# Kernel optimization log

Hardware: AMD Instinct MI355X
Metric: run time of the kernel (lower is better)

## Reference

```python
import jax, jax.numpy as jnp
import numpy as np

B, T, S, H, V, L = 64, 60, 60, 512, 32000, 2
NEG = -1.0e9  # matches torch mask value -1000000000.0


def setup_inputs() -> dict:
    key = jax.random.key(0)
    ks = jax.random.split(key, 12)
    sc = 0.05
    return {
        "indices": jax.random.randint(ks[0], (B, T), 0, V),
        "enc_output": jax.random.normal(ks[1], (B, S, H), dtype=jnp.float32),
        "de_lens": jax.random.randint(ks[2], (B,), 1, S + 1),
        "emb": jax.random.normal(ks[3], (V, H), dtype=jnp.float32) * sc,
        "w_ih": jax.random.normal(ks[4], (L, 4 * H, H), dtype=jnp.float32) * sc,
        "w_hh": jax.random.normal(ks[5], (L, 4 * H, H), dtype=jnp.float32) * sc,
        "b_ih": jnp.zeros((L, 4 * H), dtype=jnp.float32),
        "b_hh": jnp.zeros((L, 4 * H), dtype=jnp.float32),
        "lin_w": jax.random.normal(ks[6], (L, H, 2 * H), dtype=jnp.float32) * sc,
        "lin_b": jnp.zeros((L, H), dtype=jnp.float32),
        "out_w": jax.random.normal(ks[7], (V, H), dtype=jnp.float32) * sc,
        "out_b": jnp.zeros((V,), dtype=jnp.float32),
    }


def _lstm_seq(x, w_ih, w_hh, b_ih, b_hh):
    # x: [B,T,H] -> hidden states [B,T,H]; torch gate order i,f,g,o
    xg = jnp.einsum('bth,gh->btg', x, w_ih) + b_ih  # [B,T,4H]
    h0 = jnp.zeros((x.shape[0], w_hh.shape[1]), x.dtype)

    def step(carry, xg_t):
        h, c = carry
        g = xg_t + h @ w_hh.T + b_hh
        i, f, gg, o = jnp.split(g, 4, axis=-1)
        c = jax.nn.sigmoid(f) * c + jax.nn.sigmoid(i) * jnp.tanh(gg)
        h = jax.nn.sigmoid(o) * jnp.tanh(c)
        return (h, c), h

    _, hs = jax.lax.scan(step, (h0, h0), jnp.swapaxes(xg, 0, 1))
    return jnp.swapaxes(hs, 0, 1)


def reference(indices, enc_output, de_lens, emb, w_ih, w_hh, b_ih, b_hh,
              lin_w, lin_b, out_w, out_b):
    # additive length mask over encoder positions: [B,S]
    mask = jnp.where(jnp.arange(S)[None, :] < de_lens[:, None], 0.0, NEG).astype(enc_output.dtype)
    x = emb[indices]  # [B,T,H]
    for l in range(L):
        dec = _lstm_seq(x, w_ih[l], w_hh[l], b_ih[l], b_hh[l])  # [B,T,H]
        scores = jnp.einsum('bth,bsh->bts', dec, enc_output) + mask[:, None, :]
        probs = jax.nn.softmax(scores, axis=-1)
        attn = jnp.einsum('bts,bsh->bth', probs, enc_output)
        cat = jnp.concatenate([dec, attn], axis=-1)  # [B,T,2H]
        x = jnp.einsum('btk,hk->bth', cat, lin_w[l]) + lin_b[l]
    return jnp.einsum('bth,vh->btv', x, out_w) + out_b  # [B,T,V]
```

## Files before the change

### kernel.cpp

```cpp
#include <hip/hip_runtime.h>
#include <hip/hip_bf16.h>
#include <math.h>

#define B_ 64
#define T_ 60
#define S_ 60
#define H_ 512
#define V_ 32000
#define L_ 2
#define BT_ (B_*T_)
#define LDSROW2 72

typedef __attribute__((ext_vector_type(8))) short short8;
typedef __attribute__((ext_vector_type(4))) float f32x4;
typedef __attribute__((ext_vector_type(4))) unsigned int u32x4;

__device__ __forceinline__ short f2bf(float x) {
  __hip_bfloat16 h = __float2bfloat16(x);
  return __builtin_bit_cast(short, h);
}
__device__ __forceinline__ float bf2f(short s) {
  unsigned int u = ((unsigned int)(unsigned short)s) << 16;
  return __builtin_bit_cast(float, u);
}
__device__ __forceinline__ float sigm(float x) { return 1.f / (1.f + __expf(-x)); }
__device__ __forceinline__ float tanh_(float x) {
  float e = __expf(-2.f * fabsf(x));
  float t = (1.f - e) / (1.f + e);
  return x >= 0.f ? t : -t;
}

__device__ __forceinline__ void ld4g(const char* p, u32x4* q, bool llc) {
  if (llc)
    asm volatile("global_load_dwordx4 %0, %4, off sc0 sc1\n\t"
                 "global_load_dwordx4 %1, %4, off offset:16 sc0 sc1\n\t"
                 "global_load_dwordx4 %2, %4, off offset:32 sc0 sc1\n\t"
                 "global_load_dwordx4 %3, %4, off offset:48 sc0 sc1"
                 : "=v"(q[0]), "=v"(q[1]), "=v"(q[2]), "=v"(q[3]) : "v"(p));
  else
    asm volatile("global_load_dwordx4 %0, %4, off sc0\n\t"
                 "global_load_dwordx4 %1, %4, off offset:16 sc0\n\t"
                 "global_load_dwordx4 %2, %4, off offset:32 sc0\n\t"
                 "global_load_dwordx4 %3, %4, off offset:48 sc0"
                 : "=v"(q[0]), "=v"(q[1]), "=v"(q[2]), "=v"(q[3]) : "v"(p));
}

#define LDSBAR() do { \
    asm volatile("s_waitcnt lgkmcnt(0)" ::: "memory"); \
    __builtin_amdgcn_s_barrier(); \
    __builtin_amdgcn_sched_barrier(0); \
  } while (0)

__global__ __launch_bounds__(256) void convbf_k(const float* __restrict__ src,
                                                short* __restrict__ dst) {
  int g = blockIdx.x * 256 + threadIdx.x;
  const float* s = src + (size_t)g * 8;
  float4 v0 = *(const float4*)s, v1 = *(const float4*)(s + 4);
  short8 o;
  o[0]=f2bf(v0.x); o[1]=f2bf(v0.y); o[2]=f2bf(v0.z); o[3]=f2bf(v0.w);
  o[4]=f2bf(v1.x); o[5]=f2bf(v1.y); o[6]=f2bf(v1.z); o[7]=f2bf(v1.w);
  *(short8*)(dst + (size_t)g * 8) = o;
}

__global__ __launch_bounds__(256) void pack_whh_k(const float* __restrict__ whh,
                                                  short* __restrict__ pk) {
  int idx = blockIdx.x * 256 + threadIdx.x;
  int l = idx >> 17, rem = idx & 131071;
  int n = rem >> 6, k8 = rem & 63;
  int g = n >> 9, j = n & 511;
  int np = (j >> 4) * 64 + g * 16 + (j & 15);
  const float* src = whh + ((size_t)l * 2048 + n) * 512 + k8 * 8;
  float4 v0 = *(const float4*)src, v1 = *(const float4*)(src + 4);
  short8 o;
  o[0]=f2bf(v0.x); o[1]=f2bf(v0.y); o[2]=f2bf(v0.z); o[3]=f2bf(v0.w);
  o[4]=f2bf(v1.x); o[5]=f2bf(v1.y); o[6]=f2bf(v1.z); o[7]=f2bf(v1.w);
  size_t dst = (size_t)l * (2048 * 512) + ((size_t)((np >> 4) * 64 + k8)) * 128 + (np & 15) * 8;
  *(short8*)(pk + dst) = o;
}

__global__ __launch_bounds__(256) void embed_k(const int* __restrict__ idx,
                                               const float* __restrict__ emb,
                                               short* __restrict__ xhi,
                                               short* __restrict__ xlo) {
  int e = blockIdx.x * 256 + threadIdx.x;
  int bt = e >> 9, h = e & (H_ - 1);
  int row = idx[bt];
  float v = emb[(size_t)row * H_ + h];
  short hi = f2bf(v);
  xhi[e] = hi;
  xlo[e] = f2bf(v - bf2f(hi));
}

template<bool XPOSE>
__global__ __launch_bounds__(256) void gemm_hl_k(
    const short* __restrict__ Ahi, const short* __restrict__ Alo,
    const short* __restrict__ Bbf,
    const float* __restrict__ bias1, const float* __restrict__ bias2,
    float* __restrict__ C, short* __restrict__ Chi, short* __restrict__ Clo,
    int M, int N, int K) {
  __shared__ short Ahs[128 * LDSROW2];
  __shared__ short Als[128 * LDSROW2];
  __shared__ short Bs[128 * LDSROW2];
  int tid = threadIdx.x;
  int bm = blockIdx.y * 128, bn = blockIdx.x * 128;
  int wid = tid >> 6, lane = tid & 63;
  int wr = wid >> 1, wc = wid & 1;
  int lrow = lane & 15;
  f32x4 acc[4][4];
#pragma unroll
  for (int i = 0; i < 4; ++i)
#pragma unroll
    for (int j = 0; j < 4; ++j) acc[i][j] = (f32x4){0.f, 0.f, 0.f, 0.f};

  int srow = tid >> 1, scol = (tid & 1) * 32;

  for (int k0 = 0; k0 < K; k0 += 64) {
    const short* ahp = Ahi + (size_t)(bm + srow) * K + k0 + scol;
    const short* alp = Alo + (size_t)(bm + srow) * K + k0 + scol;
    const short* bp  = Bbf + (size_t)(bn + srow) * K + k0 + scol;
#pragma unroll
    for (int u = 0; u < 4; ++u) {
      *(short8*)(Ahs + srow * LDSROW2 + scol + u * 8) = *(const short8*)(ahp + u * 8);
      *(short8*)(Als + srow * LDSROW2 + scol + u * 8) = *(const short8*)(alp + u * 8);
      *(short8*)(Bs  + srow * LDSROW2 + scol + u * 8) = *(const short8*)(bp  + u * 8);
    }
    __syncthreads();
#pragma unroll
    for (int kk = 0; kk < 2; ++kk) {
      int lk = kk * 32 + (lane >> 4) * 8;
      short8 ah[4], al[4], bfr[4];
#pragma unroll
      for (int i = 0; i < 4; ++i) {
        ah[i] = *(const short8*)(Ahs + (wr * 64 + i * 16 + lrow) * LDSROW2 + lk);
        al[i] = *(const short8*)(Als + (wr * 64 + i * 16 + lrow) * LDSROW2 + lk);
      }
#pragma unroll
      for (int j = 0; j < 4; ++j)
        bfr[j] = *(const short8*)(Bs + (wc * 64 + j * 16 + lrow) * LDSROW2 + lk);
#pragma unroll
      for (int i = 0; i < 4; ++i)
#pragma unroll
        for (int j = 0; j < 4; ++j) {
          acc[i][j] = __builtin_amdgcn_mfma_f32_16x16x32_bf16(ah[i], bfr[j], acc[i][j], 0, 0, 0);
          acc[i][j] = __builtin_amdgcn_mfma_f32_16x16x32_bf16(al[i], bfr[j], acc[i][j], 0, 0, 0);
        }
    }
    __syncthreads();
  }

#pragma unroll
  for (int j = 0; j < 4; ++j) {
    int col = bn + wc * 64 + j * 16 + lrow;
    float bv = bias1[col] + (bias2 ? bias2[col] : 0.f);
#pragma unroll
    for (int i = 0; i < 4; ++i) {
#pragma unroll
      for (int r = 0; r < 4; ++r) {
        int row = bm + wr * 64 + i * 16 + (lane >> 4) * 4 + r;
        float v = acc[i][j][r] + bv;
        if (XPOSE) {
          int b = row / T_, t = row - b * T_;
          int g = col >> 9, jg = col & 511;
          int c8 = b >> 3, bloc = b & 7, q = jg >> 6;
          int nploc = ((jg >> 4) & 3) * 64 + g * 16 + (jg & 15);
          C[(((size_t)t * 64 + q * 8 + c8) * 8 + bloc) * 256 + nploc] = v;
        } else {
          short hi = f2bf(v);
          Chi[(size_t)row * N + col] = hi;
          Clo[(size_t)row * N + col] = f2bf(v - bf2f(hi));
        }
      }
    }
  }
}

__global__ __launch_bounds__(256) void gemm_bb_k(
    const short* __restrict__ A, const short* __restrict__ Bbf,
    const float* __restrict__ bias, float* __restrict__ C) {
  const int N = V_, K = H_;
  int n = blockIdx.x;
  int xcd = n & 7, pos = n >> 3;
  int base = (xcd < 4) ? xcd * 938 : 4 * 938 + (xcd - 4) * 937;
  int wg = base + pos;
  int bm = (wg % 30) * 128;
  int bn = (wg / 30) * 128;

  __shared__ short As[128 * LDSROW2];
  __shared__ short Bs[128 * LDSROW2];
  int tid = threadIdx.x;
  int wid = tid >> 6, lane = tid & 63;
  int wr = wid >> 1, wc = wid & 1;
  int lrow = lane & 15;
  f32x4 acc[4][4];
#pragma unroll
  for (int i = 0; i < 4; ++i)
#pragma unroll
    for (int j = 0; j < 4; ++j) acc[i][j] = (f32x4){0.f, 0.f, 0.f, 0.f};

  int srow = tid >> 2, scol = (tid & 3) * 16;

  for (int k0 = 0; k0 < K; k0 += 64) {
#pragma unroll
    for (int it = 0; it < 2; ++it) {
      int r = srow + it * 64;
      const short* ap = A + (size_t)(bm + r) * K + k0 + scol;
      short8 a0 = *(const short8*)ap, a1 = *(const short8*)(ap + 8);
      *(short8*)(As + r * LDSROW2 + scol) = a0;
      *(short8*)(As + r * LDSROW2 + scol + 8) = a1;
      const short* bp = Bbf + (size_t)(bn + r) * K + k0 + scol;
      short8 b0 = *(const short8*)bp, b1 = *(const short8*)(bp + 8);
      *(short8*)(Bs + r * LDSROW2 + scol) = b0;
      *(short8*)(Bs + r * LDSROW2 + scol + 8) = b1;
    }
    __syncthreads();
#pragma unroll
    for (int kk = 0; kk < 2; ++kk) {
      int lk = kk * 32 + (lane >> 4) * 8;
      short8 af[4], bfr[4];
#pragma unroll
      for (int i = 0; i < 4; ++i)
        af[i] = *(const short8*)(As + (wr * 64 + i * 16 + lrow) * LDSROW2 + lk);
#pragma unroll
      for (int j = 0; j < 4; ++j)
        bfr[j] = *(const short8*)(Bs + (wc * 64 + j * 16 + lrow) * LDSROW2 + lk);
#pragma unroll
      for (int i = 0; i < 4; ++i)
#pragma unroll
        for (int j = 0; j < 4; ++j)
          acc[i][j] = __builtin_amdgcn_mfma_f32_16x16x32_bf16(af[i], bfr[j], acc[i][j], 0, 0, 0);
    }
    __syncthreads();
  }

#pragma unroll
  for (int j = 0; j < 4; ++j) {
    int col = bn + wc * 64 + j * 16 + lrow;
    float bv = bias[col];
#pragma unroll
    for (int i = 0; i < 4; ++i)
#pragma unroll
      for (int r = 0; r < 4; ++r) {
        int row = bm + wr * 64 + i * 16 + (lane >> 4) * 4 + r;
        float v = acc[i][j][r] + bv;
        float* cp = C + (size_t)row * N + col;
        asm volatile("global_store_dword %0, %1, off nt" :: "v"(cp), "v"(v) : "memory");
      }
  }
}

__global__ __launch_bounds__(512, 2) void lstm_seq_k(
    const float* __restrict__ xg,
    const short* __restrict__ whh_pk,
    char* __restrict__ hx,
    float* __restrict__ dec) {
  __shared__ short hhi[16][520];
  __shared__ short hlo[16][520];
  __shared__ float gates[256][20];
  const int tid = threadIdx.x;
  const int bid = blockIdx.x;
  const int c = bid & 7, q = bid >> 3;
  const int w = tid >> 6, lane = tid & 63;
  const int lr = lane & 15, lkg = lane >> 4;

  for (int i = tid; i < 16 * 520; i += 512) {
    ((short*)hhi)[i] = 0;
    ((short*)hlo)[i] = 0;
  }

  short8 wreg[2][16];
#pragma unroll
  for (int nt = 0; nt < 2; ++nt)
#pragma unroll
    for (int kt = 0; kt < 16; ++kt)
      wreg[nt][kt] = *(const short8*)(whh_pk +
          ((size_t)((q * 16 + w * 2 + nt) * 64 + kt * 4 + lkg)) * 128 + lr * 8);

  const bool epi = (tid < 256);
  const int bloc_e = tid & 7;
  const int p_e = (tid >> 3) & 31;
  const int j0 = p_e * 2;
  const int s = tid & 255;
  char* grp = hx + (size_t)c * 65536;

  float cc0 = 0.f, cc1 = 0.f;
  __syncthreads();

  for (int t = 0; t < T_; ++t) {
    const unsigned tgt = (unsigned)t;
    float2 xgv[4];
    const int rw0 = (j0 >> 4) * 64 + (j0 & 15);
    if (epi) {
      const float* xb = xg + ((size_t)t * 64 + bid) * 2048 + bloc_e * 256;
#pragma unroll
      for (int g = 0; g < 4; ++g) xgv[g] = *(const float2*)(xb + rw0 + g * 16);
      asm volatile("" ::: "memory");
    } else {
      const char* base = grp + (size_t)(t & 1) * 32768;
      const char* pA = base + (size_t)s * 64;
      const char* pB = base + (size_t)(s + 256) * 64;
      u32x4 qA[4], qB[4];
      ld4g(pA, qA, true);
      ld4g(pB, qB, true);
      for (;;) {
        asm volatile("s_waitcnt vmcnt(0)" ::: "memory");
        __builtin_amdgcn_sched_barrier(0);
        unsigned bad = 0;
#pragma unroll
        for (int i = 0; i < 4; ++i) bad |= (qA[i][2] ^ tgt) | (qB[i][2] ^ tgt);
        if (!bad) break;
        __builtin_amdgcn_s_sleep(1);
        ld4g(pA, qA, true);
        ld4g(pB, qB, true);
      }
      u32x4 hA = {qA[0][0], qA[1][0], qA[2][0], qA[3][0]};
      u32x4 lA = {qA[0][1], qA[1][1], qA[2][1], qA[3][1]};
      u32x4 hB = {qB[0][0], qB[1][0], qB[2][0], qB[3][0]};
      u32x4 lB = {qB[0][1], qB[1][1], qB[2][1], qB[3][1]};
      *(u32x4*)(&hhi[s >> 6][(s & 63) * 8]) = hA;
      *(u32x4*)(&hlo[s >> 6][(s & 63) * 8]) = lA;
      *(u32x4*)(&hhi[4 + (s >> 6)][(s & 63) * 8]) = hB;
      *(u32x4*)(&hlo[4 + (s >> 6)][(s & 63) * 8]) = lB;
    }
    LDSBAR();

    f32x4 acc[2];
    acc[0] = (f32x4){0.f, 0.f, 0.f, 0.f};
    acc[1] = (f32x4){0.f, 0.f, 0.f, 0.f};
#pragma unroll
    for (int kt = 0; kt < 16; ++kt) {
      short8 ah = *(const short8*)(&hhi[lr][kt * 32 + lkg * 8]);
      short8 al = *(const short8*)(&hlo[lr][kt * 32 + lkg * 8]);
#pragma unroll
      for (int nt = 0; nt < 2; ++nt) {
        acc[nt] = __builtin_amdgcn_mfma_f32_16x16x32_bf16(ah, wreg[nt][kt], acc[nt], 0, 0, 0);
        acc[nt] = __builtin_amdgcn_mfma_f32_16x16x32_bf16(al, wreg[nt][kt], acc[nt], 0, 0, 0);
      }
    }
#pragma unroll
    for (int nt = 0; nt < 2; ++nt)
      *(f32x4*)(&gates[(w * 2 + nt) * 16 + lr][lkg * 4]) = acc[nt];
    LDSBAR();

    if (epi) {
      float gv0[4], gv1[4];
#pragma unroll
      for (int g = 0; g < 4; ++g) {
        int rw = rw0 + g * 16;
        gv0[g] = gates[rw][bloc_e] + xgv[g].x;
        gv1[g] = gates[rw + 1][bloc_e] + xgv[g].y;
      }
      float cn0 = sigm(gv0[1]) * cc0 + sigm(gv0[0]) * tanh_(gv0[2]);
      float hn0 = sigm(gv0[3]) * tanh_(cn0);
      cc0 = cn0;
      float cn1 = sigm(gv1[1]) * cc1 + sigm(gv1[0]) * tanh_(gv1[2]);
      float hn1 = sigm(gv1[3]) * tanh_(cn1);
      cc1 = cn1;
      short hi0 = f2bf(hn0), hi1 = f2bf(hn1);
      short lo0 = f2bf(hn0 - bf2f(hi0)), lo1 = f2bf(hn1 - bf2f(hi1));
      u32x4 hv;
      hv[0] = (unsigned)(unsigned short)hi0 | ((unsigned)(unsigned short)hi1 << 16);
      hv[1] = (unsigned)(unsigned short)lo0 | ((unsigned)(unsigned short)lo1 << 16);
      hv[2] = tgt + 1u;
      hv[3] = tgt + 1u;
      char* pb = grp + (size_t)((t + 1) & 1) * 32768 +
                 ((size_t)(bloc_e * 256 + q * 32 + p_e)) * 16;
      asm volatile("global_store_dwordx4 %0, %1, off sc0" :: "v"(pb), "v"(hv) : "memory");
      asm volatile("global_store_dwordx4 %0, %1, off sc0 sc1" :: "v"(pb), "v"(hv) : "memory");
      float2 dv; dv.x = hn0; dv.y = hn1;
      *(float2*)(dec + ((size_t)(c * 8 + bloc_e) * T_ + t) * H_ + q * 64 + j0) = dv;
    }
    LDSBAR();
  }
}

__global__ __launch_bounds__(256) void attn_k(const float* __restrict__ dec,
                                              const float* __restrict__ enc,
                                              const int* __restrict__ lens,
                                              short* __restrict__ cat_hi,
                                              short* __restrict__ cat_lo) {
  int bt = blockIdx.x;
  int b = bt / T_;
  __shared__ float dsh[H_];
  __shared__ float p[64];
  int tid = threadIdx.x;
  dsh[tid] = dec[(size_t)bt * H_ + tid];
  dsh[tid + 256] = dec[(size_t)bt * H_ + tid + 256];
  __syncthreads();
  int wid = tid >> 6, lane = tid & 63;
  int len = lens[b];
  for (int s = wid; s < S_; s += 4) {
    const float* er = enc + ((size_t)(b * S_ + s)) * H_ + lane * 8;
    float4 e0 = *(const float4*)er, e1 = *(const float4*)(er + 4);
    const float* dr = dsh + lane * 8;
    float sum = e0.x*dr[0] + e0.y*dr[1] + e0.z*dr[2] + e0.w*dr[3]
              + e1.x*dr[4] + e1.y*dr[5] + e1.z*dr[6] + e1.w*dr[7];
#pragma unroll
    for (int off = 32; off > 0; off >>= 1) sum += __shfl_down(sum, off);
    if (lane == 0) p[s] = sum + (s < len ? 0.f : -1.0e9f);
  }
  __syncthreads();
  if (wid == 0) {
    float v = (lane < S_) ? p[lane] : -INFINITY;
    float m = v;
#pragma unroll
    for (int off = 32; off > 0; off >>= 1) m = fmaxf(m, __shfl_down(m, off));
    m = __shfl(m, 0);
    float e = (lane < S_) ? expf(v - m) : 0.f;
    float ssum = e;
#pragma unroll
    for (int off = 32; off > 0; off >>= 1) ssum += __shfl_down(ssum, off);
    ssum = __shfl(ssum, 0);
    if (lane < S_) p[lane] = e / ssum;
  }
  __syncthreads();
  int h = tid * 2;
  float a0 = 0.f, a1 = 0.f;
  for (int s = 0; s < S_; ++s) {
    float ps = p[s];
    const float* er = enc + ((size_t)(b * S_ + s)) * H_ + h;
    a0 += ps * er[0];
    a1 += ps * er[1];
  }
  size_t base = (size_t)bt * (2 * H_);
  float vv[4] = {dsh[h], dsh[h + 1], a0, a1};
  int   oo[4] = {h, h + 1, H_ + h, H_ + h + 1};
#pragma unroll
  for (int i = 0; i < 4; ++i) {
    short hi = f2bf(vv[i]);
    cat_hi[base + oo[i]] = hi;
    cat_lo[base + oo[i]] = f2bf(vv[i] - bf2f(hi));
  }
}

extern "C" void kernel_launch(void* const* d_in, const int* in_sizes, int n_in,
                              void* d_out, int out_size, void* d_ws, size_t ws_size,
                              hipStream_t stream) {
  (void)in_sizes; (void)n_in; (void)out_size; (void)ws_size;
  const int*   indices = (const int*)d_in[0];
  const float* enc     = (const float*)d_in[1];
  const int*   de_lens = (const int*)d_in[2];
  const float* emb     = (const float*)d_in[3];
  const float* w_ih    = (const float*)d_in[4];
  const float* w_hh    = (const float*)d_in[5];
  const float* b_ih    = (const float*)d_in[6];
  const float* b_hh    = (const float*)d_in[7];
  const float* lin_w   = (const float*)d_in[8];
  const float* lin_b   = (const float*)d_in[9];
  const float* out_w   = (const float*)d_in[10];
  const float* out_b   = (const float*)d_in[11];
  float* outp = (float*)d_out;

  char* ws = (char*)d_ws;
  size_t off = 0;
  auto alloc = [&](size_t bytes) -> void* {
    void* p = ws + off; off += (bytes + 255) & ~(size_t)255; return p;
  };
  short* x_hi   = (short*)alloc((size_t)BT_ * H_ * 2);
  short* x_lo   = (short*)alloc((size_t)BT_ * H_ * 2);
  float* xg     = (float*)alloc((size_t)BT_ * 4 * H_ * 4);
  float* dec    = (float*)alloc((size_t)BT_ * H_ * 4);
  short* cat_hi = (short*)alloc((size_t)BT_ * 2 * H_ * 2);
  short* cat_lo = (short*)alloc((size_t)BT_ * 2 * H_ * 2);
  short* ow_bf  = (short*)alloc((size_t)V_ * H_ * 2);
  short* wih_bf = (short*)alloc((size_t)L_ * 4 * H_ * H_ * 2);
  short* linw_bf= (short*)alloc((size_t)L_ * H_ * 2 * H_ * 2);
  short* whh_pk = (short*)alloc((size_t)L_ * 4 * H_ * H_ * 2);
  char*  hx     = (char*)alloc((size_t)8 * 2 * 32768);

  convbf_k<<<V_ * H_ / 8 / 256, 256, 0, stream>>>(out_w, ow_bf);
  convbf_k<<<L_ * 4 * H_ * H_ / 8 / 256, 256, 0, stream>>>(w_ih, wih_bf);
  convbf_k<<<L_ * H_ * 2 * H_ / 8 / 256, 256, 0, stream>>>(lin_w, linw_bf);
  pack_whh_k<<<L_ * 2048 * 64 / 256, 256, 0, stream>>>(w_hh, whh_pk);
  embed_k<<<BT_ * H_ / 256, 256, 0, stream>>>(indices, emb, x_hi, x_lo);

  for (int l = 0; l < L_; ++l) {
    gemm_hl_k<true><<<dim3(4 * H_ / 128, BT_ / 128), 256, 0, stream>>>(
        x_hi, x_lo, wih_bf + (size_t)l * 4 * H_ * H_,
        b_ih + l * 4 * H_, b_hh + l * 4 * H_,
        xg, nullptr, nullptr, BT_, 4 * H_, H_);
    hipMemsetAsync(hx, 0, (size_t)8 * 2 * 32768, stream);
    lstm_seq_k<<<64, 512, 0, stream>>>(
        xg, whh_pk + (size_t)l * 4 * H_ * H_, hx, dec);
    attn_k<<<BT_, 256, 0, stream>>>(dec, enc, de_lens, cat_hi, cat_lo);
    gemm_hl_k<false><<<dim3(H_ / 128, BT_ / 128), 256, 0, stream>>>(
        cat_hi, cat_lo, linw_bf + (size_t)l * H_ * 2 * H_,
        lin_b + l * H_, nullptr,
        nullptr, x_hi, x_lo, BT_, H_, 2 * H_);
  }

  gemm_bb_k<<<30 * (V_ / 128), 256, 0, stream>>>(x_hi, ow_bf, out_b, outp);
}
```

Measured before the change: 964.3 us.

## Stage GEMM tiles via direct global-to-LDS loads with K-step of 32

Both bf16 MFMA GEMM kernels now copy A and B tiles straight from global memory into LDS using the global_load_lds builtin instead of loading into registers and storing. The K step drops from 64 to 32 and the padded LDS row stride of 72 becomes an unpadded stride of 32. This is meant to cut register traffic and VGPR pressure in the staging path. In exchange there are twice as many barrier pairs per K loop, and the unpadded layout may cause LDS bank conflicts on fragment reads.

Measured after the change: 979.9 us. About the same (+1.6%).

```diff
diff --git a/kernel.cpp b/kernel.cpp
--- a/kernel.cpp
+++ b/kernel.cpp
@@ -9,7 +9,6 @@
 #define V_ 32000
 #define L_ 2
 #define BT_ (B_*T_)
-#define LDSROW2 72
 
 typedef __attribute__((ext_vector_type(8))) short short8;
 typedef __attribute__((ext_vector_type(4))) float f32x4;
@@ -28,6 +27,12 @@
   float e = __expf(-2.f * fabsf(x));
   float t = (1.f - e) / (1.f + e);
   return x >= 0.f ? t : -t;
+}
+
+__device__ __forceinline__ void gll16(const short* g, short* l) {
+  __builtin_amdgcn_global_load_lds(
+      (const __attribute__((address_space(1))) void*)g,
+      (__attribute__((address_space(3))) void*)l, 16, 0, 0);
 }
 
 __device__ __forceinline__ void ld4g(const char* p, u32x4* q, bool llc) {
@@ -98,53 +103,52 @@
     const float* __restrict__ bias1, const float* __restrict__ bias2,
     float* __restrict__ C, short* __restrict__ Chi, short* __restrict__ Clo,
     int M, int N, int K) {
-  __shared__ short Ahs[128 * LDSROW2];
-  __shared__ short Als[128 * LDSROW2];
-  __shared__ short Bs[128 * LDSROW2];
+  __shared__ short Ahs[128 * 32];
+  __shared__ short Als[128 * 32];
+  __shared__ short Bs[128 * 32];
   int tid = threadIdx.x;
   int bm = blockIdx.y * 128, bn = blockIdx.x * 128;
   int wid = tid >> 6, lane = tid & 63;
   int wr = wid >> 1, wc = wid & 1;
-  int lrow = lane & 15;
+  int lrow = lane & 15, lk = (lane >> 4) * 8;
   f32x4 acc[4][4];
 #pragma unroll
   for (int i = 0; i < 4; ++i)
 #pragma unroll
     for (int j = 0; j < 4; ++j) acc[i][j] = (f32x4){0.f, 0.f, 0.f, 0.f};
 
-  int srow = tid >> 1, scol = (tid & 1) * 32;
-
-  for (int k0 = 0; k0 < K; k0 += 64) {
-    const short* ahp = Ahi + (size_t)(bm + srow) * K + k0 + scol;
-    const short* alp = Alo + (size_t)(bm + srow) * K + k0 + scol;
-    const short* bp  = Bbf + (size_t)(bn + srow) * K + k0 + scol;
-#pragma unroll
-    for (int u = 0; u < 4; ++u) {
-      *(short8*)(Ahs + srow * LDSROW2 + scol + u * 8) = *(const short8*)(ahp + u * 8);
-      *(short8*)(Als + srow * LDSROW2 + scol + u * 8) = *(const short8*)(alp + u * 8);
-      *(short8*)(Bs  + srow * LDSROW2 + scol + u * 8) = *(const short8*)(bp  + u * 8);
+  const short* gAh = Ahi + (size_t)(bm + wid * 32 + (lane >> 2)) * K + (lane & 3) * 8;
+  const short* gAl = Alo + (size_t)(bm + wid * 32 + (lane >> 2)) * K + (lane & 3) * 8;
+  const short* gB  = Bbf + (size_t)(bn + wid * 32 + (lane >> 2)) * K + (lane & 3) * 8;
+  short* lAh = Ahs + wid * 1024;
+  short* lAl = Als + wid * 1024;
+  short* lB  = Bs  + wid * 1024;
+  const size_t r16 = (size_t)16 * K;
+
+  for (int k0 = 0; k0 < K; k0 += 32) {
+    gll16(gAh + k0, lAh);
+    gll16(gAh + k0 + r16, lAh + 512);
+    gll16(gAl + k0, lAl);
+    gll16(gAl + k0 + r16, lAl + 512);
+    gll16(gB + k0, lB);
+    gll16(gB + k0 + r16, lB + 512);
+    __syncthreads();
+    short8 ah[4], al[4], bfr[4];
+#pragma unroll
+    for (int i = 0; i < 4; ++i) {
+      ah[i] = *(const short8*)(Ahs + (wr * 64 + i * 16 + lrow) * 32 + lk);
+      al[i] = *(const short8*)(Als + (wr * 64 + i * 16 + lrow) * 32 + lk);
     }
-    __syncthreads();
-#pragma unroll
-    for (int kk = 0; kk < 2; ++kk) {
-      int lk = kk * 32 + (lane >> 4) * 8;
-      short8 ah[4], al[4], bfr[4];
-#pragma unroll
-      for (int i = 0; i < 4; ++i) {
-        ah[i] = *(const short8*)(Ahs + (wr * 64 + i * 16 + lrow) * LDSROW2 + lk);
-        al[i] = *(const short8*)(Als + (wr * 64 + i * 16 + lrow) * LDSROW2 + lk);
-      }
-#pragma unroll
-      for (int j = 0; j < 4; ++j)
-        bfr[j] = *(const short8*)(Bs + (wc * 64 + j * 16 + lrow) * LDSROW2 + lk);
-#pragma unroll
-      for (int i = 0; i < 4; ++i)
-#pragma unroll
-        for (int j = 0; j < 4; ++j) {
-          acc[i][j] = __builtin_amdgcn_mfma_f32_16x16x32_bf16(ah[i], bfr[j], acc[i][j], 0, 0, 0);
-          acc[i][j] = __builtin_amdgcn_mfma_f32_16x16x32_bf16(al[i], bfr[j], acc[i][j], 0, 0, 0);
-        }
-    }
+#pragma unroll
+    for (int j = 0; j < 4; ++j)
+      bfr[j] = *(const short8*)(Bs + (wc * 64 + j * 16 + lrow) * 32 + lk);
+#pragma unroll
+    for (int i = 0; i < 4; ++i)
+#pragma unroll
+      for (int j = 0; j < 4; ++j) {
+        acc[i][j] = __builtin_amdgcn_mfma_f32_16x16x32_bf16(ah[i], bfr[j], acc[i][j], 0, 0, 0);
+        acc[i][j] = __builtin_amdgcn_mfma_f32_16x16x32_bf16(al[i], bfr[j], acc[i][j], 0, 0, 0);
+      }
     __syncthreads();
   }
 
@@ -185,50 +189,42 @@
   int bm = (wg % 30) * 128;
   int bn = (wg / 30) * 128;
 
-  __shared__ short As[128 * LDSROW2];
-  __shared__ short Bs[128 * LDSROW2];
+  __shared__ short As[128 * 32];
+  __shared__ short Bs[128 * 32];
   int tid = threadIdx.x;
   int wid = tid >> 6, lane = tid & 63;
   int wr = wid >> 1, wc = wid & 1;
-  int lrow = lane & 15;
+  int lrow = lane & 15, lk = (lane >> 4) * 8;
   f32x4 acc[4][4];
 #pragma unroll
   for (int i = 0; i < 4; ++i)
 #pragma unroll
     for (int j = 0; j < 4; ++j) acc[i][j] = (f32x4){0.f, 0.f, 0.f, 0.f};
 
-  int srow = tid >> 2, scol = (tid & 3) * 16;
-
-  for (int k0 = 0; k0 < K; k0 += 64) {
-#pragma unroll
-    for (int it = 0; it < 2; ++it) {
-      int r = srow + it * 64;
-      const short* ap = A + (size_t)(bm + r) * K + k0 + scol;
-      short8 a0 = *(const short8*)ap, a1 = *(const short8*)(ap + 8);
-      *(short8*)(As + r * LDSROW2 + scol) = a0;
-      *(short8*)(As + r * LDSROW2 + scol + 8) = a1;
-      const short* bp = Bbf + (size_t)(bn + r) * K + k0 + scol;
-      short8 b0 = *(const short8*)bp, b1 = *(const short8*)(bp + 8);
-      *(short8*)(Bs + r * LDSROW2 + scol) = b0;
-      *(short8*)(Bs + r * LDSROW2 + scol + 8) = b1;
-    }
+  const short* gA = A + (size_t)(bm + wid * 32 + (lane >> 2)) * K + (lane & 3) * 8;
+  const short* gB = Bbf + (size_t)(bn + wid * 32 + (lane >> 2)) * K + (lane & 3) * 8;
+  short* lA = As + wid * 1024;
+  short* lB = Bs + wid * 1024;
+  const size_t r16 = (size_t)16 * K;
+
+  for (int k0 = 0; k0 < K; k0 += 32) {
+    gll16(gA + k0, lA);
+    gll16(gA + k0 + r16, lA + 512);
+    gll16(gB + k0, lB);
+    gll16(gB + k0 + r16, lB + 512);
     __syncthreads();
-#pragma unroll
-    for (int kk = 0; kk < 2; ++kk) {
-      int lk = kk * 32 + (lane >> 4) * 8;
-      short8 af[4], bfr[4];
-#pragma unroll
-      for (int i = 0; i < 4; ++i)
-        af[i] = *(const short8*)(As + (wr * 64 + i * 16 + lrow) * LDSROW2 + lk);
+    short8 af[4], bfr[4];
+#pragma unroll
+    for (int i = 0; i < 4; ++i)
+      af[i] = *(const short8*)(As + (wr * 64 + i * 16 + lrow) * 32 + lk);
+#pragma unroll
+    for (int j = 0; j < 4; ++j)
+      bfr[j] = *(const short8*)(Bs + (wc * 64 + j * 16 + lrow) * 32 + lk);
+#pragma unroll
+    for (int i = 0; i < 4; ++i)
 #pragma unroll
       for (int j = 0; j < 4; ++j)
-        bfr[j] = *(const short8*)(Bs + (wc * 64 + j * 16 + lrow) * LDSROW2 + lk);
-#pragma unroll
-      for (int i = 0; i < 4; ++i)
-#pragma unroll
-        for (int j = 0; j < 4; ++j)
-          acc[i][j] = __builtin_amdgcn_mfma_f32_16x16x32_bf16(af[i], bfr[j], acc[i][j], 0, 0, 0);
-    }
+        acc[i][j] = __builtin_amdgcn_mfma_f32_16x16x32_bf16(af[i], bfr[j], acc[i][j], 0, 0, 0);
     __syncthreads();
   }
 
```
